# Optimization experiments

Measured on AMD Instinct MI355X. Metric: run time of the kernel, lower is better.

The kernel has to match this reference:

```python
import jax, jax.numpy as jnp
import numpy as np


def setup_inputs() -> dict:
    key = jax.random.key(0)
    ks = jax.random.split(key, 4)
    B, T, Z, FV = 128, 16, 33, 28 * 28
    return {
        "img": jax.random.uniform(ks[0], (B, 28, 28), dtype=jnp.float32),
        "whz": 0.05 * jax.random.normal(ks[1], (T, Z, FV), dtype=jnp.float32),
        "bias": 0.05 * jax.random.normal(ks[2], (1,), dtype=jnp.float32),
        "b_scale_out": jnp.zeros((), dtype=jnp.float32),
        "prior_tzz": 0.5 * jax.random.normal(ks[3], (T, Z, Z), dtype=jnp.float32),
        "M": 8,
        "nstep": 4,
    }


def reference(img, whz, bias, b_scale_out, prior_tzz, M, nstep):
    B = img.shape[0]
    T, Z, FV = whz.shape
    K = Z - 1
    x = img.reshape(B, FV)  # node_bx, treated as constant (detached in original)
    # disjoint pixel segments per latent slot t (partition [0, FV))
    sep = FV // T + 1
    vv = jnp.arange(FV)
    tt = jnp.arange(T)
    mask_tl = (vv[None, :] >= tt[:, None] * sep) & (vv[None, :] < (tt[:, None] + 1) * sep)  # (T, FV)
    scale = jnp.exp(b_scale_out)
    loc = whz + bias[0]  # (T, Z, FV)
    # Gaussian log-likelihood of each pixel under each (slot t, state z): (T, Z, B, FV)
    diff = (x[None, None, :, :] - loc[:, :, None, :]) / scale
    logn = -0.5 * diff * diff - jnp.log(scale) - 0.5 * jnp.log(2.0 * jnp.pi)
    # per-slot segment likelihood table lp_seg[t, z, b] = sum over pixels owned by slot t
    lp_seg = jnp.einsum('tzbv,tv->tzb', logn, mask_tl.astype(logn.dtype))  # (T, Z, B)
    lp_prior_log = jax.nn.log_softmax(prior_tzz, axis=-1)  # (T, Z, Z)

    t_idx = tt
    b_idx = jnp.arange(B)
    kk = jnp.arange(K)
    base_key = jax.random.key(42)

    def step(carry, i):
        xmz, lp_m = carry  # xmz: (B, M, T) int, lp_m: (B, M)
        t = i % T
        # K candidate assignments: copy of xmz with slot t replaced by k
        xkz = jnp.broadcast_to(xmz[:, :, None, :], (B, M, K, T))
        xkz = xkz.at[:, :, :, t].set(kk[None, None, :])
        # external (pixel) log-likelihood: sum_t lp_seg[t, z_t, b]
        lp_ext = lp_seg[t_idx[None, None, None, :], xkz, b_idx[:, None, None, None]].sum(-1)  # (B, M, K)
        # internal (Markov-chain prior), parent of slot 0 is state 0
        parents = jnp.concatenate([jnp.zeros((B, M, K, 1), xkz.dtype), xkz[..., :-1]], axis=-1)
        lp_int = lp_prior_log[t_idx[None, None, None, :], parents, xkz].sum(-1)  # (B, M, K)
        lp_total = lp_ext + lp_int
        idx_k = jax.random.categorical(jax.random.fold_in(base_key, i), lp_total, axis=-1)  # (B, M)
        lp_m = jnp.take_along_axis(lp_total, idx_k[..., None], axis=-1)[..., 0]
        xmz = xmz.at[:, :, t].set(idx_k)
        return (xmz, lp_m), None

    xmz0 = jnp.zeros((B, M, T), dtype=jnp.int32)
    lp_m0 = jnp.zeros((B, M), dtype=x.dtype)
    (xmz, lp_m), _ = jax.lax.scan(step, (xmz0, lp_m0), jnp.arange(nstep * T))
    lse = jax.nn.logsumexp(lp_m, axis=-1)  # (B,)
    return -lse.mean()
```

## Files before the change

### kernel.cpp

```cpp
#include <hip/hip_runtime.h>
#include <cstdint>

#define T_ 16
#define Z_ 33
#define K_ 32
#define FV_ 784
#define B_ 128
#define M_ 8
#define NSTEP_ 4
#define SEP_ 50
#define NOISE_N (64u * 32768u)

#define GN_OFF    0u
#define LPSEG_OFF 2097152u
#define PLW_OFF   (LPSEG_OFF + 67584u)
#define LPM_OFF   (PLW_OFF + 17424u)
#define WS_NEED_BYTES ((size_t)(LPM_OFF + 1024u + 16u) * 4)

__device__ __forceinline__ uint32_t rotl32(uint32_t v, int r) {
  return (v << r) | (v >> (32 - r));
}

__device__ __forceinline__ void tf2x32(uint32_t k0, uint32_t k1,
                                       uint32_t& x0, uint32_t& x1) {
  uint32_t k2 = k0 ^ k1 ^ 0x1BD11BDAu;
  x0 += k0; x1 += k1;
#define RND_(r) { x0 += x1; x1 = rotl32(x1, r); x1 ^= x0; }
  RND_(13) RND_(15) RND_(26) RND_(6)
  x0 += k1; x1 += k2 + 1u;
  RND_(17) RND_(29) RND_(16) RND_(24)
  x0 += k2; x1 += k0 + 2u;
  RND_(13) RND_(15) RND_(26) RND_(6)
  x0 += k0; x1 += k1 + 3u;
  RND_(17) RND_(29) RND_(16) RND_(24)
  x0 += k1; x1 += k2 + 4u;
  RND_(13) RND_(15) RND_(26) RND_(6)
  x0 += k2; x1 += k0 + 5u;
#undef RND_
}

__device__ __forceinline__ float gumbel_fast(uint32_t bits) {
  const float TINY = 1.17549435e-38f;
  float u = __uint_as_float((bits >> 9) | 0x3F800000u) - 1.0f;
  u = fmaxf(TINY, u * (1.0f - TINY) + TINY);
  return -__logf(-__logf(u));
}

__device__ __forceinline__ float gumbel_bits(uint32_t bits) {
  const float TINY = 1.17549435e-38f;
  float u = __uint_as_float((bits >> 9) | 0x3F800000u) - 1.0f;
  u = fmaxf(TINY, u * (1.0f - TINY) + TINY);
  return -logf(-logf(u));
}

template <int CTRL>
__device__ __forceinline__ float dpp_f(float x) {
  int xi = __float_as_int(x);
  int r = __builtin_amdgcn_update_dpp(xi, xi, CTRL, 0xF, 0xF, false);
  return __int_as_float(r);
}


__global__ __launch_bounds__(256) void ZBML3_noise(float* __restrict__ gn) {
  const uint32_t g = (uint32_t)(blockIdx.x * 256 + threadIdx.x);
  const uint32_t i = g >> 12;
  const uint32_t jb = g & 4095u;
  uint32_t k0 = 0u, k1 = i;
  tf2x32(0u, 42u, k0, k1);
  float* out = gn + (size_t)i * 32768u;
#pragma unroll
  for (uint32_t jj = 0; jj < 4; ++jj) {
    uint32_t j = jb + jj * 4096u;
    uint32_t x0 = j, x1 = j + 16384u;
    tf2x32(k0, k1, x0, x1);
    out[j] = gumbel_fast(x0);
    out[j + 16384u] = gumbel_fast(x1);
  }
}

__global__ __launch_bounds__(256) void ZBML3_tables(
    const float* __restrict__ img, const float* __restrict__ whz,
    const float* __restrict__ bias_p, const float* __restrict__ bso_p,
    const float* __restrict__ prior, float* __restrict__ ws) {
  const int bid = blockIdx.x, tid = threadIdx.x;
  float* lpseg = ws + LPSEG_OFF;
  float* plw = ws + PLW_OFF;
  if (bid < 528) {
    const int e = bid;
    if (tid < B_) {
      const int b = tid;
      const float bias0 = bias_p[0];
      const float scale = expf(bso_p[0]);
      const float con = -logf(scale) - 0.9189385332046727f;
      const int t = e / 33;
      const int v0 = t * SEP_;
      const int v1 = (v0 + SEP_ < FV_) ? v0 + SEP_ : FV_;
      const float* wp = whz + (size_t)e * FV_;
      const float* xp = img + (size_t)b * FV_;
      float acc = 0.0f;
      for (int v = v0; v < v1; ++v) {
        float d = (xp[v] - (wp[v] + bias0)) / scale;
        acc += -0.5f * d * d;
      }
      lpseg[b * 528 + e] = acc + (float)(v1 - v0) * con;
    }
  } else {
    const int r = (bid - 528) * 256 + tid;
    if (r < 528) {
      const float* pr = prior + r * 33;
      float mx = pr[0];
      for (int z = 1; z < 33; ++z) mx = fmaxf(mx, pr[z]);
      float sse = 0.0f;
      for (int z = 0; z < 33; ++z) sse += __expf(pr[z] - mx);
      float lg = __logf(sse);
      for (int z = 0; z < 33; ++z) plw[r * 33 + z] = pr[z] - mx - lg;
    }
  }
}

__global__ __launch_bounds__(256) void ZBML3_gibbs5(
    const float* __restrict__ gn, const float* __restrict__ lpseg,
    const float* __restrict__ plw_g, float* __restrict__ lpm) {
  __shared__ float pl[T_ * 1089];
  __shared__ float sseg[528];

  const int b = blockIdx.x;
  const int tid = threadIdx.x;
  const int k = tid & 31;
  const int m = tid >> 5;
  const int half = m & 1;
  const uint32_t idx = (uint32_t)(b * 256 + tid);

  {
    const float4* src = (const float4*)plw_g;
    float4* dst = (float4*)pl;
#pragma unroll
    for (int it = 0; it < 17; ++it) {
      int j = it * 256 + tid;
      if (j < 4356) dst[j] = src[j];
    }
    const float4* ss = (const float4*)(lpseg + b * 528);
    float4* dd = (float4*)sseg;
    if (tid < 132) dd[tid] = ss[tid];
  }

  float g0[T_];
#pragma unroll
  for (int t = 0; t < T_; ++t) g0[t] = gn[(size_t)t * 32768u + idx];

  __syncthreads();

  float sl[T_];
#pragma unroll
  for (int t = 0; t < T_; ++t) sl[t] = sseg[t * 33 + k];

  int s[T_];
#pragma unroll
  for (int t = 0; t < T_; ++t) s[t] = 0;

  float c[T_];
#pragma unroll
  for (int t = 0; t < T_; ++t) {
    float pn = (t < T_ - 1) ? pl[(t + 1) * 1089 + k * 33] : 0.0f;
    c[t] = g0[t] + sl[t] + pn;
  }

#pragma unroll
  for (int w = 0; w < NSTEP_; ++w) {
    if (w < NSTEP_ - 1) {
#pragma unroll
      for (int t = 0; t < T_; ++t)
        g0[t] = gn[(size_t)((w + 1) * 16 + t) * 32768u + idx];
    }
#pragma unroll
    for (int t = 0; t < T_; ++t) {
      const int p = (t == 0) ? 0 : s[t - 1];
      float v = c[t] + pl[t * 1089 + p * 33 + k];
      float rm = v;
      rm = fmaxf(rm, dpp_f<0x121>(rm));
      rm = fmaxf(rm, dpp_f<0x122>(rm));
      rm = fmaxf(rm, dpp_f<0x124>(rm));
      rm = fmaxf(rm, dpp_f<0x128>(rm));
      float bc = dpp_f<0x142>(rm);
      float m2 = fmaxf(rm, bc);
      int mAi = __builtin_amdgcn_readlane(__float_as_int(m2), 31);
      int mBi = __builtin_amdgcn_readlane(__float_as_int(m2), 63);
      float vmax = __int_as_float(half == 0 ? mAi : mBi);
      unsigned long long ball = __ballot(v == vmax);
      int kA = __ffs((unsigned int)ball) - 1;
      int kB = __ffs((unsigned int)(ball >> 32)) - 1;
      s[t] = (half == 0) ? kA : kB;
    }
    if (w < NSTEP_ - 1) {
#pragma unroll
      for (int t = 0; t < T_; ++t) {
        float pn = (t < T_ - 1) ? pl[(t + 1) * 1089 + k * 33 + s[t + 1]] : 0.0f;
        c[t] = g0[t] + sl[t] + pn;
      }
    }
  }

  float lpf = 0.0f;
  int prev = 0;
#pragma unroll
  for (int t = 0; t < T_; ++t) {
    lpf += sseg[t * 33 + s[t]] + pl[t * 1089 + prev * 33 + s[t]];
    prev = s[t];
  }
  if (k == 0) lpm[b * 8 + m] = lpf;
}

__global__ __launch_bounds__(128) void ZBML3_final(
    const float* __restrict__ lpm, float* __restrict__ out) {
  __shared__ float sm[B_];
  const int tid = threadIdx.x;
  const float* lp = lpm + tid * 8;
  float mx = lp[0];
#pragma unroll
  for (int mm = 1; mm < M_; ++mm) mx = fmaxf(mx, lp[mm]);
  float sse = 0.0f;
#pragma unroll
  for (int mm = 0; mm < M_; ++mm) sse += __expf(lp[mm] - mx);
  sm[tid] = mx + __logf(sse);
  __syncthreads();
  if (tid == 0) {
    float s = 0.0f;
    for (int i = 0; i < B_; ++i) s += sm[i];
    out[0] = -(s * (1.0f / 128.0f));
  }
}


__global__ __launch_bounds__(256) void ZBML3_gibbs_kernel(
    const float* __restrict__ img, const float* __restrict__ whz,
    const float* __restrict__ bias_p, const float* __restrict__ bso_p,
    const float* __restrict__ prior, float* __restrict__ lse_out) {
  __shared__ float pl[T_ * Z_ * Z_];
  __shared__ float slseg[T_ * Z_];
  __shared__ float xrow[FV_];
  __shared__ uint32_t key0s[NSTEP_ * T_], key1s[NSTEP_ * T_];
  __shared__ float lpm[M_];

  const int b = blockIdx.x;
  const int tid = threadIdx.x;
  const float bias0 = bias_p[0];
  const float scale = expf(bso_p[0]);
  const float con = -logf(scale) - 0.9189385332046727f;

  for (int v = tid; v < FV_; v += 256) xrow[v] = img[b * FV_ + v];
  __syncthreads();

  for (int e = tid; e < T_ * Z_; e += 256) {
    int t = e / Z_;
    int v0 = t * SEP_;
    int v1 = v0 + SEP_ < FV_ ? v0 + SEP_ : FV_;
    float acc = 0.0f;
    const float* wp = whz + (size_t)e * FV_;
    for (int v = v0; v < v1; ++v) {
      float d = (xrow[v] - (wp[v] + bias0)) / scale;
      acc += -0.5f * d * d;
    }
    slseg[e] = acc + (float)(v1 - v0) * con;
  }
  for (int r = tid; r < T_ * Z_; r += 256) {
    const float* pr = prior + r * Z_;
    float mx = pr[0];
    for (int z = 1; z < Z_; ++z) mx = fmaxf(mx, pr[z]);
    float sse = 0.0f;
    for (int z = 0; z < Z_; ++z) sse += expf(pr[z] - mx);
    float lg = logf(sse);
    for (int z = 0; z < Z_; ++z) pl[r * Z_ + z] = pr[z] - mx - lg;
  }
  if (tid < NSTEP_ * T_) {
    uint32_t x0 = 0u, x1 = (uint32_t)tid;
    tf2x32(0u, 42u, x0, x1);
    key0s[tid] = x0; key1s[tid] = x1;
  }
  __syncthreads();

  const int m = tid >> 5;
  const int k = tid & 31;
  const uint32_t idx = (uint32_t)(b * 256 + tid);
  const uint32_t jctr = idx & 16383u;
  const bool sel0 = idx < 16384u;

  int s[T_];
#pragma unroll
  for (int t = 0; t < T_; ++t) s[t] = 0;

  for (int sweep = 0; sweep < NSTEP_; ++sweep) {
#pragma unroll
    for (int t = 0; t < T_; ++t) {
      const int i = sweep * T_ + t;
      const uint32_t kk0 = key0s[i], kk1 = key1s[i];
      const int p = (t == 0) ? 0 : s[t - 1];
      float lp = slseg[t * Z_ + k] + pl[t * Z_ * Z_ + p * Z_ + k];
      if (t < T_ - 1) lp += pl[(t + 1) * Z_ * Z_ + k * Z_ + s[t + 1]];
      uint32_t x0 = jctr, x1 = jctr + 16384u;
      tf2x32(kk0, kk1, x0, x1);
      float g = gumbel_bits(sel0 ? x0 : x1);
      float val = lp + g;
      int ki = k;
      for (int d = 16; d > 0; d >>= 1) {
        float ov = __shfl_xor(val, d);
        int oi = __shfl_xor(ki, d);
        if (ov > val || (ov == val && oi < ki)) { val = ov; ki = oi; }
      }
      s[t] = ki;
    }
  }

  float lpf = 0.0f;
  int prev = 0;
#pragma unroll
  for (int t = 0; t < T_; ++t) {
    lpf += slseg[t * Z_ + s[t]] + pl[t * Z_ * Z_ + prev * Z_ + s[t]];
    prev = s[t];
  }
  if (k == 0) lpm[m] = lpf;
  __syncthreads();
  if (tid == 0) {
    float mx = lpm[0];
    for (int mm = 1; mm < M_; ++mm) mx = fmaxf(mx, lpm[mm]);
    float sse = 0.0f;
    for (int mm = 0; mm < M_; ++mm) sse += expf(lpm[mm] - mx);
    lse_out[b] = mx + logf(sse);
  }
}

__global__ __launch_bounds__(128) void ZBML3_reduce_kernel(
    const float* __restrict__ lse, float* __restrict__ out) {
  __shared__ float sm[B_];
  const int tid = threadIdx.x;
  sm[tid] = lse[tid];
  __syncthreads();
  if (tid == 0) {
    float s = 0.0f;
    for (int i = 0; i < B_; ++i) s += sm[i];
    out[0] = -(s / (float)B_);
  }
}

extern "C" void kernel_launch(void* const* d_in, const int* in_sizes, int n_in,
                              void* d_out, int out_size, void* d_ws, size_t ws_size,
                              hipStream_t stream) {
  const float* img   = (const float*)d_in[0];
  const float* whz   = (const float*)d_in[1];
  const float* bias  = (const float*)d_in[2];
  const float* bso   = (const float*)d_in[3];
  const float* prior = (const float*)d_in[4];

  if (ws_size >= WS_NEED_BYTES) {
    float* ws = (float*)d_ws;
    ZBML3_noise<<<1024, 256, 0, stream>>>(ws + GN_OFF);
    ZBML3_tables<<<531, 256, 0, stream>>>(img, whz, bias, bso, prior, ws);
    ZBML3_gibbs5<<<B_, 256, 0, stream>>>(ws + GN_OFF, ws + LPSEG_OFF,
                                         ws + PLW_OFF, ws + LPM_OFF);
    ZBML3_final<<<1, 128, 0, stream>>>(ws + LPM_OFF, (float*)d_out);
  } else {
    float* lse = (float*)d_ws;
    ZBML3_gibbs_kernel<<<B_, 256, 0, stream>>>(img, whz, bias, bso, prior, lse);
    ZBML3_reduce_kernel<<<1, B_, 0, stream>>>(lse, (float*)d_out);
  }
}
```

Measured before the change: 39.38 us.

## Fuse noise generation, table building and Gibbs sampling into one kernel

```diff
diff --git a/kernel.cpp b/kernel.cpp
--- a/kernel.cpp
+++ b/kernel.cpp
@@ -9,13 +9,8 @@
 #define M_ 8
 #define NSTEP_ 4
 #define SEP_ 50
-#define NOISE_N (64u * 32768u)
-
-#define GN_OFF    0u
-#define LPSEG_OFF 2097152u
-#define PLW_OFF   (LPSEG_OFF + 67584u)
-#define LPM_OFF   (PLW_OFF + 17424u)
-#define WS_NEED_BYTES ((size_t)(LPM_OFF + 1024u + 16u) * 4)
+
+#define WS_NEED_BYTES ((size_t)(1024 + 16) * 4)
 
 __device__ __forceinline__ uint32_t rotl32(uint32_t v, int r) {
   return (v << r) | (v >> (32 - r));
@@ -60,99 +55,79 @@
   return __int_as_float(r);
 }
 
-
-__global__ __launch_bounds__(256) void ZBML3_noise(float* __restrict__ gn) {
-  const uint32_t g = (uint32_t)(blockIdx.x * 256 + threadIdx.x);
-  const uint32_t i = g >> 12;
-  const uint32_t jb = g & 4095u;
-  uint32_t k0 = 0u, k1 = i;
-  tf2x32(0u, 42u, k0, k1);
-  float* out = gn + (size_t)i * 32768u;
-#pragma unroll
-  for (uint32_t jj = 0; jj < 4; ++jj) {
-    uint32_t j = jb + jj * 4096u;
-    uint32_t x0 = j, x1 = j + 16384u;
-    tf2x32(k0, k1, x0, x1);
-    out[j] = gumbel_fast(x0);
-    out[j + 16384u] = gumbel_fast(x1);
-  }
-}
-
-__global__ __launch_bounds__(256) void ZBML3_tables(
+__global__ __launch_bounds__(256) void ZBML3_fused(
     const float* __restrict__ img, const float* __restrict__ whz,
     const float* __restrict__ bias_p, const float* __restrict__ bso_p,
-    const float* __restrict__ prior, float* __restrict__ ws) {
-  const int bid = blockIdx.x, tid = threadIdx.x;
-  float* lpseg = ws + LPSEG_OFF;
-  float* plw = ws + PLW_OFF;
-  if (bid < 528) {
-    const int e = bid;
-    if (tid < B_) {
-      const int b = tid;
-      const float bias0 = bias_p[0];
-      const float scale = expf(bso_p[0]);
-      const float con = -logf(scale) - 0.9189385332046727f;
+    const float* __restrict__ prior, float* __restrict__ lpm) {
+  __shared__ float pl[T_ * 1089];
+  __shared__ float gnl[64 * 256];
+  __shared__ float sseg[528];
+  __shared__ uint32_t key0s[64], key1s[64];
+
+  const int b = blockIdx.x;
+  const int tid = threadIdx.x;
+  const int k = tid & 31;
+  const int m = tid >> 5;
+  const int half = m & 1;
+
+  if (tid < 64) {
+    uint32_t x0 = 0u, x1 = (uint32_t)tid;
+    tf2x32(0u, 42u, x0, x1);
+    key0s[tid] = x0; key1s[tid] = x1;
+  }
+
+  {
+    const float bias0 = bias_p[0];
+    const float scale = expf(bso_p[0]);
+    const float con = -logf(scale) - 0.9189385332046727f;
+    const float* xp = img + (size_t)b * FV_;
+    for (int e = tid; e < 528; e += 256) {
       const int t = e / 33;
       const int v0 = t * SEP_;
       const int v1 = (v0 + SEP_ < FV_) ? v0 + SEP_ : FV_;
       const float* wp = whz + (size_t)e * FV_;
-      const float* xp = img + (size_t)b * FV_;
       float acc = 0.0f;
       for (int v = v0; v < v1; ++v) {
         float d = (xp[v] - (wp[v] + bias0)) / scale;
         acc += -0.5f * d * d;
       }
-      lpseg[b * 528 + e] = acc + (float)(v1 - v0) * con;
-    }
-  } else {
-    const int r = (bid - 528) * 256 + tid;
-    if (r < 528) {
-      const float* pr = prior + r * 33;
-      float mx = pr[0];
-      for (int z = 1; z < 33; ++z) mx = fmaxf(mx, pr[z]);
-      float sse = 0.0f;
-      for (int z = 0; z < 33; ++z) sse += __expf(pr[z] - mx);
-      float lg = __logf(sse);
-      for (int z = 0; z < 33; ++z) plw[r * 33 + z] = pr[z] - mx - lg;
-    }
-  }
-}
-
-__global__ __launch_bounds__(256) void ZBML3_gibbs5(
-    const float* __restrict__ gn, const float* __restrict__ lpseg,
-    const float* __restrict__ plw_g, float* __restrict__ lpm) {
-  __shared__ float pl[T_ * 1089];
-  __shared__ float sseg[528];
-
-  const int b = blockIdx.x;
-  const int tid = threadIdx.x;
-  const int k = tid & 31;
-  const int m = tid >> 5;
-  const int half = m & 1;
-  const uint32_t idx = (uint32_t)(b * 256 + tid);
+      sseg[e] = acc + (float)(v1 - v0) * con;
+    }
+  }
+
+  for (int r = tid; r < 528; r += 256) {
+    const float* pr = prior + r * 33;
+    float mx = pr[0];
+    for (int z = 1; z < 33; ++z) mx = fmaxf(mx, pr[z]);
+    float sse = 0.0f;
+    for (int z = 0; z < 33; ++z) sse += __expf(pr[z] - mx);
+    float lg = __logf(sse);
+    for (int z = 0; z < 33; ++z) pl[r * 33 + z] = pr[z] - mx - lg;
+  }
+
+  __syncthreads();
 
   {
-    const float4* src = (const float4*)plw_g;
-    float4* dst = (float4*)pl;
-#pragma unroll
-    for (int it = 0; it < 17; ++it) {
-      int j = it * 256 + tid;
-      if (j < 4356) dst[j] = src[j];
-    }
-    const float4* ss = (const float4*)(lpseg + b * 528);
-    float4* dd = (float4*)sseg;
-    if (tid < 132) dd[tid] = ss[tid];
-  }
+    const uint32_t idx = (uint32_t)(b * 256 + tid);
+    const uint32_t j0 = idx & 16383u;
+    const bool sel0 = idx < 16384u;
+#pragma unroll 4
+    for (int i = 0; i < 64; ++i) {
+      uint32_t x0 = j0, x1 = j0 + 16384u;
+      tf2x32(key0s[i], key1s[i], x0, x1);
+      gnl[i * 256 + tid] = gumbel_fast(sel0 ? x0 : x1);
+    }
+  }
+
+  __syncthreads();
+
+  float sl[T_];
+#pragma unroll
+  for (int t = 0; t < T_; ++t) sl[t] = sseg[t * 33 + k];
 
   float g0[T_];
 #pragma unroll
-  for (int t = 0; t < T_; ++t) g0[t] = gn[(size_t)t * 32768u + idx];
-
-  __syncthreads();
-
-  float sl[T_];
-#pragma unroll
-  for (int t = 0; t < T_; ++t) sl[t] = sseg[t * 33 + k];
+  for (int t = 0; t < T_; ++t) g0[t] = gnl[t * 256 + tid];
 
   int s[T_];
 #pragma unroll
@@ -170,7 +145,7 @@
     if (w < NSTEP_ - 1) {
 #pragma unroll
       for (int t = 0; t < T_; ++t)
-        g0[t] = gn[(size_t)((w + 1) * 16 + t) * 32768u + idx];
+        g0[t] = gnl[((w + 1) * 16 + t) * 256 + tid];
     }
 #pragma unroll
     for (int t = 0; t < T_; ++t) {
@@ -351,12 +326,9 @@
   const float* prior = (const float*)d_in[4];
 
   if (ws_size >= WS_NEED_BYTES) {
-    float* ws = (float*)d_ws;
-    ZBML3_noise<<<1024, 256, 0, stream>>>(ws + GN_OFF);
-    ZBML3_tables<<<531, 256, 0, stream>>>(img, whz, bias, bso, prior, ws);
-    ZBML3_gibbs5<<<B_, 256, 0, stream>>>(ws + GN_OFF, ws + LPSEG_OFF,
-                                         ws + PLW_OFF, ws + LPM_OFF);
-    ZBML3_final<<<1, 128, 0, stream>>>(ws + LPM_OFF, (float*)d_out);
+    float* lpm = (float*)d_ws;
+    ZBML3_fused<<<B_, 256, 0, stream>>>(img, whz, bias, bso, prior, lpm);
+    ZBML3_final<<<1, 128, 0, stream>>>(lpm, (float*)d_out);
   } else {
     float* lse = (float*)d_ws;
     ZBML3_gibbs_kernel<<<B_, 256, 0, stream>>>(img, whz, bias, bso, prior, lse);
```

Result: slower. 55.27 us (+40.4%).
